# Optimization experiments

Measured on AMD Instinct MI355X. Metric: run time of the kernel, lower is better.

The kernel has to match this reference:

```python
import jax, jax.numpy as jnp
import numpy as np

B, D = 32, 512
N_IMG, N_KN = 50000, 8192
C = 32          # num_classes
R = 16          # image_retrieval_number
K = 8           # knowledge_retrieval_number
NEG = -1e9


def setup_inputs() -> dict:
    key = jax.random.key(0)
    k1, k2, k3, k4, k5 = jax.random.split(key, 5)
    return {
        'query_embeddings': jax.random.normal(k1, (B, D), dtype=jnp.float32),
        'all_image_embeddings': jax.random.normal(k2, (N_IMG, D), dtype=jnp.float32),
        'all_knowledge_embeddings': jax.random.normal(k3, (N_KN, D), dtype=jnp.float32),
        'image_labels': jax.random.randint(k4, (N_IMG,), 0, C, dtype=jnp.int32),
        'knowledge_labels': jax.random.randint(k5, (N_KN,), 0, C, dtype=jnp.int32),
    }


def reference(query_embeddings, all_image_embeddings, all_knowledge_embeddings,
              image_labels, knowledge_labels):
    classes = jnp.arange(C, dtype=jnp.int32)
    img_class_mask = image_labels[None, :] == classes[:, None]       # [C, N_img]
    kn_class_mask = knowledge_labels[None, :] == classes[:, None]    # [C, N_kn]

    # per-class masked similarity retrieval of images
    sims = query_embeddings @ all_image_embeddings.T                 # [B, N_img]
    masked = jnp.where(img_class_mask[None], sims[:, None, :], NEG)  # [B, C, N_img]
    img_vals, img_idx = jax.lax.top_k(masked, R)                     # [B, C, R]
    img_w = jax.nn.softmax(img_vals, axis=-1)
    similar_images = all_image_embeddings[img_idx]                   # [B, C, R, D]

    # image fusion (average of query and attention-weighted retrieved context)
    fused_img = jnp.einsum('bcr,bcrd->bcd', img_w, similar_images)
    enhanced_images = 0.5 * (query_embeddings[:, None, :] + fused_img)  # [B, C, D]

    # class-masked knowledge retrieval for every retrieved image
    ksims = jnp.einsum('bcrd,nd->bcrn', similar_images, all_knowledge_embeddings)
    kmasked = jnp.where(kn_class_mask[None, :, None, :], ksims, NEG)  # [B, C, R, N_kn]
    k_vals, k_idx = jax.lax.top_k(kmasked, K)                         # [B, C, R, K]
    k_w = jax.nn.softmax(k_vals, axis=-1)
    selected_knowledge = all_knowledge_embeddings[k_idx]              # [B, C, R, K, D]

    # knowledge fusion: weight over K, then over R with image weights, average w/ query
    fused_k = jnp.einsum('bcrk,bcrkd->bcrd', k_w, selected_knowledge)
    fused_k = jnp.einsum('bcr,bcrd->bcd', img_w, fused_k)
    enhanced_knowledge = 0.5 * (query_embeddings[:, None, :] + fused_k)  # [B, C, D]

    return enhanced_images, enhanced_knowledge
```

## Files before the change

### kernel.cpp

```cpp
#include <hip/hip_runtime.h>
#include <math.h>

#define NIMG 50000
#define NKN  8192
#define BB   32
#define DD   512
#define CC   32
#define RR   16
#define KK   8
#define MMAX 384

typedef float f4v __attribute__((ext_vector_type(4)));

__global__ __launch_bounds__(256) void build_lists(const int* __restrict__ labels,
                                                   int n, int* __restrict__ cnt,
                                                   int* __restrict__ list, int stride) {
    int i = blockIdx.x * 256 + threadIdx.x;
    if (i < n) {
        int c = labels[i];
        int pos = atomicAdd(&cnt[c], 1);
        list[c * stride + pos] = i;
    }
}

__global__ __launch_bounds__(256) void sims_kernel(const float* __restrict__ Q,
                                                   const float* __restrict__ I,
                                                   float* __restrict__ S) {
    __shared__ float4 qs[BB * DD / 4];
    for (int i = threadIdx.x; i < BB * DD / 4; i += 256)
        qs[i] = ((const float4*)Q)[i];
    __syncthreads();
    int n = blockIdx.x * 256 + threadIdx.x;
    if (n >= NIMG) return;
    float acc[BB];
#pragma unroll
    for (int b = 0; b < BB; b++) acc[b] = 0.f;
    const float4* row = (const float4*)(I + (size_t)n * DD);
    for (int d4 = 0; d4 < DD / 4; d4++) {
        float4 v = row[d4];
#pragma unroll
        for (int b = 0; b < BB; b++) {
            float4 q = qs[b * (DD / 4) + d4];
            acc[b] += v.x * q.x + v.y * q.y + v.z * q.z + v.w * q.w;
        }
    }
#pragma unroll
    for (int b = 0; b < BB; b++) S[(size_t)b * NIMG + n] = acc[b];
}

__global__ __launch_bounds__(256) void topk_img(const float* __restrict__ S,
                                                const int* __restrict__ cnt,
                                                const int* __restrict__ list,
                                                int* __restrict__ t_idx,
                                                float* __restrict__ t_w) {
    int c = blockIdx.x, b = blockIdx.y, tid = threadIdx.x;
    __shared__ float sval[256 * RR];
    __shared__ int   sidx[256 * RR];
    __shared__ float redv[256];
    __shared__ int   redp[256];
    __shared__ float kv[RR];
    __shared__ int   ki[RR];

    float tv[RR]; int ti[RR];
#pragma unroll
    for (int k = 0; k < RR; k++) { tv[k] = -1e30f; ti[k] = 0; }

    int m = cnt[c];
    for (int j = tid; j < m; j += 256) {
        int n = list[c * NIMG + j];
        float v = S[(size_t)b * NIMG + n];
        if (v > tv[RR - 1]) {
            int p = RR - 1;
            while (p > 0 && tv[p - 1] < v) { tv[p] = tv[p - 1]; ti[p] = ti[p - 1]; p--; }
            tv[p] = v; ti[p] = n;
        }
    }
#pragma unroll
    for (int k = 0; k < RR; k++) { sval[tid * RR + k] = tv[k]; sidx[tid * RR + k] = ti[k]; }
    __syncthreads();

    for (int k = 0; k < RR; k++) {
        float bv = -1e30f; int bp = 0;
        for (int j = tid; j < 256 * RR; j += 256)
            if (sval[j] > bv) { bv = sval[j]; bp = j; }
        redv[tid] = bv; redp[tid] = bp;
        __syncthreads();
        for (int s = 128; s > 0; s >>= 1) {
            if (tid < s && redv[tid + s] > redv[tid]) { redv[tid] = redv[tid + s]; redp[tid] = redp[tid + s]; }
            __syncthreads();
        }
        if (tid == 0) { kv[k] = redv[0]; ki[k] = sidx[redp[0]]; sval[redp[0]] = -1e30f; }
        __syncthreads();
    }

    if (tid == 0) {
        float mx = kv[0], s = 0.f, e[RR];
#pragma unroll
        for (int k = 0; k < RR; k++) { e[k] = expf(kv[k] - mx); s += e[k]; }
        float inv = 1.f / s;
        size_t o = ((size_t)(b * CC) + c) * RR;
#pragma unroll
        for (int k = 0; k < RR; k++) { t_w[o + k] = e[k] * inv; t_idx[o + k] = ki[k]; }
    }
}

__global__ __launch_bounds__(256) void img_kernel(const float* __restrict__ Q,
                                                  const float* __restrict__ I,
                                                  const int* __restrict__ t_idx,
                                                  const float* __restrict__ t_w,
                                                  float* __restrict__ out) {
    int c = blockIdx.x, b = blockIdx.y, tid = threadIdx.x;
    __shared__ float w[RR];
    __shared__ int   id[RR];
    if (tid < RR) {
        size_t o = ((size_t)(b * CC) + c) * RR;
        w[tid] = t_w[o + tid]; id[tid] = t_idx[o + tid];
    }
    __syncthreads();
    for (int d = tid; d < DD; d += 256) {
        float acc = 0.f;
#pragma unroll
        for (int r = 0; r < RR; r++) acc += w[r] * I[(size_t)id[r] * DD + d];
        out[((size_t)(b * CC) + c) * DD + d] = 0.5f * (Q[b * DD + d] + acc);
    }
}

__global__ __launch_bounds__(256) void transpose_kn(const float* __restrict__ KN,
                                                    const int* __restrict__ kcnt,
                                                    const int* __restrict__ klist,
                                                    float4* __restrict__ KT4) {
    int c = blockIdx.x;
    int w = threadIdx.x >> 6, lane = threadIdx.x & 63;
    int j = blockIdx.y * 4 + w;
    int m = kcnt[c]; if (m > MMAX) m = MMAX;
    int row = klist[c * NKN + (j < m ? j : 0)];
    const float4* src = (const float4*)(KN + (size_t)row * DD);
    float4* dst = KT4 + (size_t)c * (DD / 4) * MMAX;
    float4 v0 = src[lane], v1 = src[lane + 64];
    dst[(size_t)lane * MMAX + j]        = v0;
    dst[(size_t)(lane + 64) * MMAX + j] = v1;
}

__global__ __launch_bounds__(256, 4) void knowledge_kernel(const float* __restrict__ Q,
                                                           const float* __restrict__ I,
                                                           const float* __restrict__ KN,
                                                           const float4* __restrict__ KT4,
                                                           const int* __restrict__ kcnt,
                                                           const int* __restrict__ klist,
                                                           const int* __restrict__ t_idx,
                                                           const float* __restrict__ t_w,
                                                           float* __restrict__ outk) {
    int c = blockIdx.x, b = blockIdx.y;
    int tid = threadIdx.x, wave = tid >> 6, lane = tid & 63;
    int rbase = wave * 4;

    __shared__ float4 simg[RR][DD / 4];
    __shared__ float  s_iw[RR];
    __shared__ int    s_ii[RR];
    __shared__ float  wgt[RR][KK];
    __shared__ int    kidx[RR][KK];

    if (tid < RR) {
        size_t o = ((size_t)(b * CC) + c) * RR;
        s_iw[tid] = t_w[o + tid]; s_ii[tid] = t_idx[o + tid];
    }
    __syncthreads();

    for (int i = tid; i < RR * DD / 4; i += 256) {
        int r = i >> 7, d4 = i & 127;
        simg[r][d4] = ((const float4*)(I + (size_t)s_ii[r] * DD))[d4];
    }

    int m = kcnt[c]; if (m > MMAX) m = MMAX;
    const float4* KTc = KT4 + (size_t)c * (DD / 4) * MMAX;

    f4v A0 = 0.f, A1 = 0.f, A2 = 0.f, A3 = 0.f, A4 = 0.f, A5 = 0.f;

    __syncthreads();

#define SC_RR(rr) { float4 u = simg[rbase + rr][d4]; \
        A0[rr] += k0.x*u.x + k0.y*u.y + k0.z*u.z + k0.w*u.w; \
        A1[rr] += k1.x*u.x + k1.y*u.y + k1.z*u.z + k1.w*u.w; \
        A2[rr] += k2.x*u.x + k2.y*u.y + k2.z*u.z + k2.w*u.w; \
        A3[rr] += k3.x*u.x + k3.y*u.y + k3.z*u.z + k3.w*u.w; \
        A4[rr] += k4.x*u.x + k4.y*u.y + k4.z*u.z + k4.w*u.w; \
        A5[rr] += k5.x*u.x + k5.y*u.y + k5.z*u.z + k5.w*u.w; }

    for (int d4 = 0; d4 < DD / 4; d4++) {
        const float4* p = KTc + (size_t)d4 * MMAX + lane;
        float4 k0 = p[0],   k1 = p[64],  k2 = p[128],
               k3 = p[192], k4 = p[256], k5 = p[320];
        SC_RR(0) SC_RR(1) SC_RR(2) SC_RR(3)
    }
#undef SC_RR

#define CAND(t) { if (!(used & (1u << t)) && \
                      (lv##t > mv || (lv##t == mv && (t * 64 + lane) < mj))) \
                  { mv = lv##t; mj = t * 64 + lane; mt = t; } }

#define ROUND(k) { \
        float mv = -1e30f; int mj = 0x7fffffff; int mt = -1; \
        CAND(0) CAND(1) CAND(2) CAND(3) CAND(4) CAND(5) \
        int cj = mj; \
        for (int off = 32; off > 0; off >>= 1) { \
            float ov = __shfl_xor(mv, off); \
            int   oj = __shfl_xor(mj, off); \
            if (ov > mv || (ov == mv && oj < mj)) { mv = ov; mj = oj; } \
        } \
        if (cj == mj && mt >= 0) used |= (1u << mt); \
        if (lane == k) myj = mj; \
        kv##k = mv; }

#define TOPK_RR(rr) { \
        int r = rbase + rr; \
        float lv0 = (0 * 64 + lane < m) ? A0[rr] : -1e30f; \
        float lv1 = (1 * 64 + lane < m) ? A1[rr] : -1e30f; \
        float lv2 = (2 * 64 + lane < m) ? A2[rr] : -1e30f; \
        float lv3 = (3 * 64 + lane < m) ? A3[rr] : -1e30f; \
        float lv4 = (4 * 64 + lane < m) ? A4[rr] : -1e30f; \
        float lv5 = (5 * 64 + lane < m) ? A5[rr] : -1e30f; \
        unsigned used = 0; int myj = 0; \
        float kv0, kv1, kv2, kv3, kv4, kv5, kv6, kv7; \
        ROUND(0) ROUND(1) ROUND(2) ROUND(3) \
        ROUND(4) ROUND(5) ROUND(6) ROUND(7) \
        if (lane < KK) kidx[r][lane] = klist[c * NKN + myj]; \
        if (lane == 0) { \
            float e0 = 1.f; \
            float e1 = expf(kv1 - kv0), e2 = expf(kv2 - kv0), e3 = expf(kv3 - kv0); \
            float e4 = expf(kv4 - kv0), e5 = expf(kv5 - kv0), e6 = expf(kv6 - kv0); \
            float e7 = expf(kv7 - kv0); \
            float s = e0 + e1 + e2 + e3 + e4 + e5 + e6 + e7; \
            float wr = s_iw[r] / s; \
            wgt[r][0] = e0 * wr; wgt[r][1] = e1 * wr; wgt[r][2] = e2 * wr; \
            wgt[r][3] = e3 * wr; wgt[r][4] = e4 * wr; wgt[r][5] = e5 * wr; \
            wgt[r][6] = e6 * wr; wgt[r][7] = e7 * wr; \
        } }

    TOPK_RR(0) TOPK_RR(1) TOPK_RR(2) TOPK_RR(3)
#undef TOPK_RR
#undef ROUND
#undef CAND

    __syncthreads();

    float acc0 = 0.f, acc1 = 0.f;
#pragma unroll 8
    for (int p = 0; p < RR * KK; p++) {
        int r = p >> 3, k = p & 7;
        float w = wgt[r][k];
        const float* kp = KN + (size_t)kidx[r][k] * DD;
        acc0 += w * kp[tid];
        acc1 += w * kp[tid + 256];
    }
    size_t o = ((size_t)(b * CC) + c) * DD;
    outk[o + tid]       = 0.5f * (Q[b * DD + tid] + acc0);
    outk[o + tid + 256] = 0.5f * (Q[b * DD + tid + 256] + acc1);
}

extern "C" void kernel_launch(void* const* d_in, const int* in_sizes, int n_in,
                              void* d_out, int out_size, void* d_ws, size_t ws_size,
                              hipStream_t stream) {
    const float* Q  = (const float*)d_in[0];
    const float* I  = (const float*)d_in[1];
    const float* KN = (const float*)d_in[2];
    const int* ilab = (const int*)d_in[3];
    const int* klab = (const int*)d_in[4];

    char* ws = (char*)d_ws;
    float* S        = (float*)ws;  ws += (size_t)BB * NIMG * 4;
    int*   img_list = (int*)ws;    ws += (size_t)CC * NIMG * 4;
    int*   kn_list  = (int*)ws;    ws += (size_t)CC * NKN * 4;
    int*   t_idx    = (int*)ws;    ws += (size_t)BB * CC * RR * 4;
    float* t_w      = (float*)ws;  ws += (size_t)BB * CC * RR * 4;
    int*   img_cnt  = (int*)ws;    ws += CC * 4;
    int*   kn_cnt   = (int*)ws;    ws += CC * 4;
    ws = (char*)(((size_t)ws + 255) & ~(size_t)255);
    float4* KT4     = (float4*)ws; ws += (size_t)CC * (DD / 4) * MMAX * 16;

    float* out_img = (float*)d_out;
    float* out_kn  = out_img + (size_t)BB * CC * DD;

    hipMemsetAsync(img_cnt, 0, 2 * CC * 4, stream);

    build_lists<<<(NIMG + 255) / 256, 256, 0, stream>>>(ilab, NIMG, img_cnt, img_list, NIMG);
    build_lists<<<(NKN  + 255) / 256, 256, 0, stream>>>(klab, NKN,  kn_cnt,  kn_list,  NKN);
    transpose_kn<<<dim3(CC, MMAX / 4), 256, 0, stream>>>(KN, kn_cnt, kn_list, KT4);
    sims_kernel<<<(NIMG + 255) / 256, 256, 0, stream>>>(Q, I, S);
    topk_img<<<dim3(CC, BB), 256, 0, stream>>>(S, img_cnt, img_list, t_idx, t_w);
    img_kernel<<<dim3(CC, BB), 256, 0, stream>>>(Q, I, t_idx, t_w, (float*)d_out);
    knowledge_kernel<<<dim3(CC, BB), 256, 0, stream>>>(Q, I, KN, KT4, kn_cnt, kn_list, t_idx, t_w, out_kn);
}
```

Baseline: 429.2 us.

## Widen knowledge kernel to 512 threads, two rows per wave, skip empty candidate groups

The knowledge kernel now runs 512 threads (8 waves), and each wave scores 2 retrieved images instead of 4. This halves the per-thread accumulator registers so more waves can be resident to hide latency. The scoring loop is specialized on the actual class population (4, 5 or 6 groups of 64 candidates), so loads and FMAs for empty groups are skipped, and the dot products now use explicit fused multiply-adds. The trade-off is that each wave re-reads the same transposed knowledge tile for fewer rows, roughly doubling global/L2 traffic per block.

```diff
diff --git a/kernel.cpp b/kernel.cpp
--- a/kernel.cpp
+++ b/kernel.cpp
@@ -10,7 +10,7 @@
 #define KK   8
 #define MMAX 384
 
-typedef float f4v __attribute__((ext_vector_type(4)));
+typedef float f2v __attribute__((ext_vector_type(2)));
 
 __global__ __launch_bounds__(256) void build_lists(const int* __restrict__ labels,
                                                    int n, int* __restrict__ cnt,
@@ -141,7 +141,7 @@
     dst[(size_t)(lane + 64) * MMAX + j] = v1;
 }
 
-__global__ __launch_bounds__(256, 4) void knowledge_kernel(const float* __restrict__ Q,
+__global__ __launch_bounds__(512, 8) void knowledge_kernel(const float* __restrict__ Q,
                                                            const float* __restrict__ I,
                                                            const float* __restrict__ KN,
                                                            const float4* __restrict__ KT4,
@@ -152,7 +152,7 @@
                                                            float* __restrict__ outk) {
     int c = blockIdx.x, b = blockIdx.y;
     int tid = threadIdx.x, wave = tid >> 6, lane = tid & 63;
-    int rbase = wave * 4;
+    int r0 = wave * 2, r1 = r0 + 1;
 
     __shared__ float4 simg[RR][DD / 4];
     __shared__ float  s_iw[RR];
@@ -166,33 +166,45 @@
     }
     __syncthreads();
 
-    for (int i = tid; i < RR * DD / 4; i += 256) {
+    for (int i = tid; i < RR * DD / 4; i += 512) {
         int r = i >> 7, d4 = i & 127;
         simg[r][d4] = ((const float4*)(I + (size_t)s_ii[r] * DD))[d4];
     }
 
     int m = kcnt[c]; if (m > MMAX) m = MMAX;
+    int ng = (m + 63) >> 6;
     const float4* KTc = KT4 + (size_t)c * (DD / 4) * MMAX;
 
-    f4v A0 = 0.f, A1 = 0.f, A2 = 0.f, A3 = 0.f, A4 = 0.f, A5 = 0.f;
-
-    __syncthreads();
-
-#define SC_RR(rr) { float4 u = simg[rbase + rr][d4]; \
-        A0[rr] += k0.x*u.x + k0.y*u.y + k0.z*u.z + k0.w*u.w; \
-        A1[rr] += k1.x*u.x + k1.y*u.y + k1.z*u.z + k1.w*u.w; \
-        A2[rr] += k2.x*u.x + k2.y*u.y + k2.z*u.z + k2.w*u.w; \
-        A3[rr] += k3.x*u.x + k3.y*u.y + k3.z*u.z + k3.w*u.w; \
-        A4[rr] += k4.x*u.x + k4.y*u.y + k4.z*u.z + k4.w*u.w; \
-        A5[rr] += k5.x*u.x + k5.y*u.y + k5.z*u.z + k5.w*u.w; }
-
-    for (int d4 = 0; d4 < DD / 4; d4++) {
-        const float4* p = KTc + (size_t)d4 * MMAX + lane;
-        float4 k0 = p[0],   k1 = p[64],  k2 = p[128],
-               k3 = p[192], k4 = p[256], k5 = p[320];
-        SC_RR(0) SC_RR(1) SC_RR(2) SC_RR(3)
-    }
-#undef SC_RR
+    f2v A0 = 0.f, A1 = 0.f, A2 = 0.f, A3 = 0.f, A4 = 0.f, A5 = 0.f;
+
+    __syncthreads();
+
+#define LG(g) float4 kk##g = p[g * 64];
+#define FG(g, rr, U) A##g[rr] = fmaf(kk##g.x, U.x, fmaf(kk##g.y, U.y, \
+                      fmaf(kk##g.z, U.z, fmaf(kk##g.w, U.w, A##g[rr]))));
+#define SCORE(LOADS, FMAS) { \
+        const float4* p = KTc + lane; \
+        for (int d4 = 0; d4 < DD / 4; d4++, p += MMAX) { \
+            LOADS \
+            float4 u0 = simg[r0][d4]; float4 u1 = simg[r1][d4]; \
+            FMAS } }
+
+    if (ng <= 4) {
+        SCORE(LG(0) LG(1) LG(2) LG(3),
+              FG(0,0,u0) FG(1,0,u0) FG(2,0,u0) FG(3,0,u0)
+              FG(0,1,u1) FG(1,1,u1) FG(2,1,u1) FG(3,1,u1))
+    } else if (ng == 5) {
+        SCORE(LG(0) LG(1) LG(2) LG(3) LG(4),
+              FG(0,0,u0) FG(1,0,u0) FG(2,0,u0) FG(3,0,u0) FG(4,0,u0)
+              FG(0,1,u1) FG(1,1,u1) FG(2,1,u1) FG(3,1,u1) FG(4,1,u1))
+    } else {
+        SCORE(LG(0) LG(1) LG(2) LG(3) LG(4) LG(5),
+              FG(0,0,u0) FG(1,0,u0) FG(2,0,u0) FG(3,0,u0) FG(4,0,u0) FG(5,0,u0)
+              FG(0,1,u1) FG(1,1,u1) FG(2,1,u1) FG(3,1,u1) FG(4,1,u1) FG(5,1,u1))
+    }
+#undef SCORE
+#undef FG
+#undef LG
 
 #define CAND(t) { if (!(used & (1u << t)) && \
                       (lv##t > mv || (lv##t == mv && (t * 64 + lane) < mj))) \
@@ -212,7 +224,7 @@
         kv##k = mv; }
 
 #define TOPK_RR(rr) { \
-        int r = rbase + rr; \
+        int r = r0 + rr; \
         float lv0 = (0 * 64 + lane < m) ? A0[rr] : -1e30f; \
         float lv1 = (1 * 64 + lane < m) ? A1[rr] : -1e30f; \
         float lv2 = (2 * 64 + lane < m) ? A2[rr] : -1e30f; \
@@ -236,25 +248,22 @@
             wgt[r][6] = e6 * wr; wgt[r][7] = e7 * wr; \
         } }
 
-    TOPK_RR(0) TOPK_RR(1) TOPK_RR(2) TOPK_RR(3)
+    TOPK_RR(0) TOPK_RR(1)
 #undef TOPK_RR
 #undef ROUND
 #undef CAND
 
     __syncthreads();
 
-    float acc0 = 0.f, acc1 = 0.f;
+    float acc0 = 0.f;
 #pragma unroll 8
     for (int p = 0; p < RR * KK; p++) {
         int r = p >> 3, k = p & 7;
         float w = wgt[r][k];
-        const float* kp = KN + (size_t)kidx[r][k] * DD;
-        acc0 += w * kp[tid];
-        acc1 += w * kp[tid + 256];
+        acc0 += w * KN[(size_t)kidx[r][k] * DD + tid];
     }
     size_t o = ((size_t)(b * CC) + c) * DD;
-    outk[o + tid]       = 0.5f * (Q[b * DD + tid] + acc0);
-    outk[o + tid + 256] = 0.5f * (Q[b * DD + tid + 256] + acc1);
+    outk[o + tid] = 0.5f * (Q[b * DD + tid] + acc0);
 }
 
 extern "C" void kernel_launch(void* const* d_in, const int* in_sizes, int n_in,
@@ -288,5 +297,5 @@
     sims_kernel<<<(NIMG + 255) / 256, 256, 0, stream>>>(Q, I, S);
     topk_img<<<dim3(CC, BB), 256, 0, stream>>>(S, img_cnt, img_list, t_idx, t_w);
     img_kernel<<<dim3(CC, BB), 256, 0, stream>>>(Q, I, t_idx, t_w, (float*)d_out);
-    knowledge_kernel<<<dim3(CC, BB), 256, 0, stream>>>(Q, I, KN, KT4, kn_cnt, kn_list, t_idx, t_w, out_kn);
-}
+    knowledge_kernel<<<dim3(CC, BB), 512, 0, stream>>>(Q, I, KN, KT4, kn_cnt, kn_list, t_idx, t_w, out_kn);
+}
```

After: 423.5 us. About the same (-1.3%).
